# Performance work log

Hardware: AMD Instinct MI355X
Metric: run time of the kernel (lower is better)

The kernel has to match this reference:

```python
import jax, jax.numpy as jnp
import numpy as np

WEIGHT = 1e-7
SIGMA_RGB = 15.0
SIGMA_XY = 100.0
SCALE = 0.5


def _nearest_resize(x, Ho, Wo):
    # torch F.interpolate mode='nearest': src = floor(dst * in/out)
    H, W = x.shape[-2], x.shape[-1]
    iy = (jnp.arange(Ho) * (H / Ho)).astype(jnp.int32)
    ix = (jnp.arange(Wo) * (W / Wo)).astype(jnp.int32)
    return x[..., iy[:, None], ix[None, :]]


def _bilinear_resize(x, Ho, Wo):
    # torch bilinear, align_corners=False (half-pixel centers, no antialias)
    H, W = x.shape[-2], x.shape[-1]
    yc = jnp.clip((jnp.arange(Ho, dtype=jnp.float32) + 0.5) * (H / Ho) - 0.5, 0.0, H - 1.0)
    xc = jnp.clip((jnp.arange(Wo, dtype=jnp.float32) + 0.5) * (W / Wo) - 0.5, 0.0, W - 1.0)
    y0 = jnp.floor(yc).astype(jnp.int32); y1 = jnp.minimum(y0 + 1, H - 1); ty = yc - y0
    x0 = jnp.floor(xc).astype(jnp.int32); x1 = jnp.minimum(x0 + 1, W - 1); tx = xc - x0
    g = lambda yi, xi: x[..., yi[:, None], xi[None, :]]
    top = g(y0, x0) * (1.0 - tx) + g(y0, x1) * tx
    bot = g(y1, x0) * (1.0 - tx) + g(y1, x1) * tx
    return top * (1.0 - ty[:, None]) + bot * ty[:, None]


def _dense_energy(images, segmentations, ROIs, seg_label):
    N, K, H, W = segmentations.shape
    Ho, Wo = int(H * SCALE), int(W * SCALE)
    P = Ho * Wo
    img_s = _nearest_resize(images, Ho, Wo)            # [N,3,Ho,Wo]
    seg_s = _bilinear_resize(segmentations, Ho, Wo)    # [N,K,Ho,Wo]
    roi_s = _nearest_resize(ROIs, Ho, Wo)              # [N,Ho,Wo]
    lbl_s = _nearest_resize(seg_label, Ho, Wo)         # [N,1,Ho,Wo]
    unlabel = (lbl_s == 255)[:, 0]                     # [N,Ho,Wo]

    # Gate = clamp(ROI - max_k seg, min=0), with unlabeled region forced to 1
    gate = roi_s - jnp.max(seg_s, axis=1)
    gate = jnp.where(unlabel, 1.0, gate)
    gate = jnp.maximum(gate, 0.0)
    gate = jax.lax.stop_gradient(gate)                 # constant in the custom backward

    seg_roi = seg_s * roi_s[:, None]                   # [N,K,Ho,Wo]

    sxy = SIGMA_XY * SCALE
    yy, xx = jnp.meshgrid(jnp.arange(Ho, dtype=jnp.float32),
                          jnp.arange(Wo, dtype=jnp.float32), indexing='ij')
    pos = jnp.stack([xx.ravel() / sxy, yy.ravel() / sxy], axis=-1)  # [P,2]

    def per_image(img, seg):
        # img [3,Ho,Wo], seg [K,Ho,Wo] -> AS [K,P]: Gaussian bilateral filter
        col = img.reshape(img.shape[0], P).T / SIGMA_RGB            # [P,3]
        f = jnp.concatenate([pos, col], axis=-1)                    # [P,5]
        sq = jnp.sum(f * f, axis=-1)
        d2 = jnp.maximum(sq[:, None] + sq[None, :] - 2.0 * (f @ f.T), 0.0)
        Wm = jnp.exp(-0.5 * d2)                                     # [P,P] affinity
        return seg.reshape(seg.shape[0], P) @ Wm                    # symmetric Wm

    AS = jax.vmap(per_image)(img_s, seg_roi)                        # [N,K,P]
    AS = AS * gate.reshape(N, 1, P)
    loss = -jnp.sum(seg_roi.reshape(N, K, P) * AS) / N
    return (WEIGHT * loss).reshape(1)


def setup_inputs() -> dict:
    key = jax.random.key(0)
    k1, k2, k3, k4 = jax.random.split(key, 4)
    N, C, K, H, W = 4, 3, 21, 128, 128
    images = jax.random.uniform(k1, (N, C, H, W), dtype=jnp.float32) * 255.0
    segmentations = jax.nn.softmax(jax.random.normal(k2, (N, K, H, W), dtype=jnp.float32), axis=1)
    ROIs = jax.random.randint(k3, (N, H, W), 0, 2).astype(jnp.float32)
    seg_label = jax.random.randint(k4, (N, 1, H, W), 0, 256).astype(jnp.int32)
    return {"images": images, "segmentations": segmentations, "ROIs": ROIs, "seg_label": seg_label}


def reference(images, segmentations, ROIs, seg_label):
    return _dense_energy(images, segmentations, ROIs, seg_label)
```

## Files before the change

### kernel.cpp

```cpp
#include <hip/hip_runtime.h>
#include <hip/hip_bf16.h>


typedef _Float16 v8h __attribute__((ext_vector_type(8)));
typedef float v16f __attribute__((ext_vector_type(16)));

#define NIMG 4
#define KCH 21
#define HIN 128
#define WIN 128
#define PPX 4096
#define TPB 32
#define TRI 528
#define NBLK (NIMG * TRI)

#define WS_S_OFF 0x000000
#define WS_F_OFF 0x180000
#define PART_OFF 0x300000

#define LOG2E 1.44269504088896341f

__device__ __forceinline__ float fexp2(float x) {
#if __has_builtin(__builtin_amdgcn_exp2f)
    return __builtin_amdgcn_exp2f(x);
#else
    return __expf(x * 0.69314718055994531f);
#endif
}

__global__ __launch_bounds__(256) void prep_kernel(
    const float* __restrict__ img, const float* __restrict__ seg,
    const float* __restrict__ roi, const int* __restrict__ lbl,
    char* __restrict__ ws)
{
    int gid = blockIdx.x * 256 + threadIdx.x;
    int n = gid >> 12, p = gid & (PPX - 1);
    int y = p >> 6, x = p & 63, iy = 2 * y, ix = 2 * x;
    const float inv_rgb = 1.0f / 15.0f, inv_sxy = 1.0f / 50.0f;

    float rv = roi[((size_t)n * HIN + iy) * WIN + ix];
    int   lb = lbl[((size_t)n * HIN + iy) * WIN + ix];

    float sv[KCH]; float maxs = 0.0f;
    #pragma unroll
    for (int k = 0; k < KCH; k++) {
        const float* sp = seg + ((((size_t)n * KCH + k) * HIN + iy) * WIN + ix);
        float2 a = *(const float2*)sp;
        float2 c = *(const float2*)(sp + WIN);
        float s = 0.25f * (a.x + a.y + c.x + c.y);
        maxs = fmaxf(maxs, s);
        sv[k] = s * rv;
    }
    float gate = (lb == 255) ? 1.0f : fmaxf(rv - maxs, 0.0f);

    union { float4 q[6]; _Float16 e[48]; } rs;
    #pragma unroll
    for (int k = 0; k < KCH; k++) {
        _Float16 s = (_Float16)sv[k];
        rs.e[k] = (_Float16)(sv[k] * gate);
        rs.e[24 + k] = s;
    }
    #pragma unroll
    for (int k = KCH; k < 24; k++) { rs.e[k] = (_Float16)0.f; rs.e[24 + k] = (_Float16)0.f; }

    float f[5];
    f[0] = (float)x * inv_sxy;
    f[1] = (float)y * inv_sxy;
    f[2] = img[(((size_t)n * 3 + 0) * HIN + iy) * WIN + ix] * inv_rgb;
    f[3] = img[(((size_t)n * 3 + 1) * HIN + iy) * WIN + ix] * inv_rgb;
    f[4] = img[(((size_t)n * 3 + 2) * HIN + iy) * WIN + ix] * inv_rgb;

    _Float16 hi[5], lo[5];
    float sq = 0.f;
    #pragma unroll
    for (int u = 0; u < 5; u++) {
        hi[u] = (_Float16)f[u];
        lo[u] = (_Float16)(f[u] - (float)hi[u]);
        float fe = (float)hi[u] + (float)lo[u];
        sq = fmaf(fe, fe, sq);
    }
    float sqv = -0.5f * sq;
    _Float16 sqh = (_Float16)sqv;
    _Float16 sql = (_Float16)(sqv - (float)sqh);
    const _Float16 h0 = (_Float16)0.f, h1 = (_Float16)1.f;

    union { float4 q[6]; _Float16 e[48]; } rf;
    #pragma unroll
    for (int u = 0; u < 5; u++) {
        rf.e[u] = hi[u];       rf.e[8 + u] = lo[u];
        rf.e[16 + u] = hi[u];  rf.e[24 + u] = hi[u];
        rf.e[32 + u] = lo[u];  rf.e[40 + u] = lo[u];
    }
    rf.e[5] = sqh; rf.e[6] = sql; rf.e[7] = h1;
    rf.e[13] = h0; rf.e[14] = h0; rf.e[15] = h1;
    rf.e[21] = h1; rf.e[22] = h1; rf.e[23] = sqh;
    rf.e[29] = h0; rf.e[30] = h0; rf.e[31] = sql;
    rf.e[37] = h0; rf.e[38] = h0; rf.e[39] = h0;
    rf.e[45] = h0; rf.e[46] = h0; rf.e[47] = h0;

    float4* ds = (float4*)(ws + WS_S_OFF + (size_t)gid * 96);
    float4* df = (float4*)(ws + WS_F_OFF + (size_t)gid * 96);
    #pragma unroll
    for (int u = 0; u < 6; u++) { ds[u] = rs.q[u]; df[u] = rf.q[u]; }
}

#define LSTR 104
#define SREG_O 0
#define FREG_O 26624
#define RED_O  53248
#define LDS_BYTES 53280

__global__ __launch_bounds__(256)
__attribute__((amdgpu_waves_per_eu(1, 4)))
void pairs_kernel(
    const char* __restrict__ ws, float* __restrict__ part)
{
    __shared__ __align__(16) char smem[LDS_BYTES];
    int b = blockIdx.x;
    int n = b / TRI, r = b - n * TRI;
    int i = 0, rowlen = TPB;
    while (r >= rowlen) { r -= rowlen; rowlen--; i++; }
    int j = i + r;
    bool diag = (i == j);

    int t = threadIdx.x;
    int lane = t & 63, half = lane >> 5, lr = lane & 31, wv = t >> 6;
    int wq = wv & 1, wp = wv >> 1;

    {
        const float4* gsi = (const float4*)(ws + WS_S_OFF) + (size_t)(n * PPX + i * 128) * 6;
        const float4* gfi = (const float4*)(ws + WS_F_OFF) + (size_t)(n * PPX + i * 128) * 6;
        #pragma unroll
        for (int k = 0; k < 3; k++) {
            int v = t + k * 256;
            int row = v / 6, off = v - row * 6;
            float4 vs = gsi[v], vf = gfi[v];
            char* dS = smem + SREG_O + row * LSTR + off * 16;
            char* dF = smem + FREG_O + row * LSTR + off * 16;
            *(float2*)dS = make_float2(vs.x, vs.y);
            *(float2*)(dS + 8) = make_float2(vs.z, vs.w);
            *(float2*)dF = make_float2(vf.x, vf.y);
            *(float2*)(dF + 8) = make_float2(vf.z, vf.w);
        }
        if (!diag) {
            const float4* gsj = (const float4*)(ws + WS_S_OFF) + (size_t)(n * PPX + j * 128) * 6;
            const float4* gfj = (const float4*)(ws + WS_F_OFF) + (size_t)(n * PPX + j * 128) * 6;
            #pragma unroll
            for (int k = 0; k < 3; k++) {
                int v = t + k * 256;
                int row = v / 6, off = v - row * 6;
                float4 vs = gsj[v], vf = gfj[v];
                char* dS = smem + SREG_O + (128 + row) * LSTR + off * 16;
                char* dF = smem + FREG_O + (128 + row) * LSTR + off * 16;
                *(float2*)dS = make_float2(vs.x, vs.y);
                *(float2*)(dS + 8) = make_float2(vs.z, vs.w);
                *(float2*)dF = make_float2(vf.x, vf.y);
                *(float2*)(dF + 8) = make_float2(vf.z, vf.w);
            }
        }
    }
    __syncthreads();

    int jrow0 = diag ? 0 : 128;
    float acc = 0.0f;

    #pragma unroll
    for (int sp = 0; sp < 2; sp++) {
        int pr = wp * 64 + sp * 32 + lr;
        const char* sb = smem + SREG_O + pr * LSTR;
        const char* fb = smem + FREG_O + pr * LSTR;
        union { v8h h; float2 f[2]; } A0, A1, A2, Af;
        A0.f[0] = *(const float2*)(sb + half * 16);
        A0.f[1] = *(const float2*)(sb + half * 16 + 8);
        A1.f[0] = *(const float2*)(sb + 32 + half * 16);
        A1.f[1] = *(const float2*)(sb + 32 + half * 16 + 8);
        A2.f[0] = *(const float2*)(sb + 64 + half * 16);
        A2.f[1] = *(const float2*)(sb + 64 + half * 16 + 8);
        Af.f[0] = *(const float2*)(fb + half * 16);
        Af.f[1] = *(const float2*)(fb + half * 16 + 8);

        #pragma unroll
        for (int s = 0; s < 2; s++) {
            int cr = jrow0 + wq * 64 + s * 32 + lr;
            const char* cb = smem + SREG_O + cr * LSTR;
            const char* gb = smem + FREG_O + cr * LSTR;
            union { v8h h; float2 f[2]; } B0, B1, B2, Bf1, Bf2;
            B0.f[0] = *(const float2*)(cb + 48 + half * 16);
            B0.f[1] = *(const float2*)(cb + 48 + half * 16 + 8);
            int o1 = half ? 0 : 80;
            B1.f[0] = *(const float2*)(cb + o1);
            B1.f[1] = *(const float2*)(cb + o1 + 8);
            B2.f[0] = *(const float2*)(cb + 16 + half * 16);
            B2.f[1] = *(const float2*)(cb + 16 + half * 16 + 8);
            Bf1.f[0] = *(const float2*)(gb + 32 + half * 16);
            Bf1.f[1] = *(const float2*)(gb + 32 + half * 16 + 8);
            Bf2.f[0] = *(const float2*)(gb + 64 + half * 16);
            Bf2.f[1] = *(const float2*)(gb + 64 + half * 16 + 8);

            v16f z = {0.f,0.f,0.f,0.f,0.f,0.f,0.f,0.f,0.f,0.f,0.f,0.f,0.f,0.f,0.f,0.f};
            v16f c2 = __builtin_amdgcn_mfma_f32_32x32x16_f16(Af.h, Bf1.h, z, 0, 0, 0);
            c2 = __builtin_amdgcn_mfma_f32_32x32x16_f16(Af.h, Bf2.h, c2, 0, 0, 0);
            v16f c1 = __builtin_amdgcn_mfma_f32_32x32x16_f16(A0.h, B0.h, z, 0, 0, 0);
            c1 = __builtin_amdgcn_mfma_f32_32x32x16_f16(A1.h, B1.h, c1, 0, 0, 0);
            c1 = __builtin_amdgcn_mfma_f32_32x32x16_f16(A2.h, B2.h, c1, 0, 0, 0);

            #pragma unroll
            for (int rr = 0; rr < 16; rr++) {
                float arg = fminf(LOG2E * c2[rr], 0.0f);
                acc = fmaf(fexp2(arg), c1[rr], acc);
            }
        }
    }

    #pragma unroll
    for (int off = 32; off > 0; off >>= 1) acc += __shfl_down(acc, off, 64);
    float* wred = (float*)(smem + RED_O);
    if ((t & 63) == 0) wred[t >> 6] = acc;
    __syncthreads();
    if (t == 0) {
        float partial = (wred[0] + wred[1]) + (wred[2] + wred[3]);
        if (diag) partial *= 0.5f;
        part[b] = partial;
    }
}

__global__ __launch_bounds__(256) void finalize_kernel(
    const float* __restrict__ part, float* __restrict__ out)
{
    __shared__ float s[256];
    int t = threadIdx.x;
    float v = 0.f;
    #pragma unroll
    for (int k = 0; k < 9; k++) {
        int idx = t + k * 256;
        if (idx < NBLK) v += part[idx];
    }
    s[t] = v;
    __syncthreads();
    #pragma unroll
    for (int off = 128; off > 0; off >>= 1) {
        if (t < off) s[t] += s[t + off];
        __syncthreads();
    }
    if (t == 0) out[0] = s[0] * (-1e-7f / (float)NIMG);
}

extern "C" void kernel_launch(void* const* d_in, const int* in_sizes, int n_in,
                              void* d_out, int out_size, void* d_ws, size_t ws_size,
                              hipStream_t stream) {
    const float* images = (const float*)d_in[0];
    const float* seg    = (const float*)d_in[1];
    const float* rois   = (const float*)d_in[2];
    const int*   lbl    = (const int*)d_in[3];
    float* out = (float*)d_out;
    char*  ws  = (char*)d_ws;
    float* part = (float*)(ws + PART_OFF);

    hipLaunchKernelGGL(prep_kernel, dim3((NIMG * PPX) / 256), dim3(256), 0, stream,
                       images, seg, rois, lbl, ws);
    hipLaunchKernelGGL(pairs_kernel, dim3(NBLK), dim3(256), 0, stream,
                       (const char*)ws, part);
    hipLaunchKernelGGL(finalize_kernel, dim3(1), dim3(256), 0, stream,
                       (const float*)part, out);
}
```

Measured before the change: 85.18 us.

## Compact feature workspace, rebuild B operands in-register, fuse finalize via last-block atomic

Shrinks the per-pixel feature record from 96 to 32 bytes, and reconstructs the two B-side feature MFMA operands in registers from the compact hi/lo rows using lane-dependent selects. This cuts global and LDS traffic and lowers the LDS footprint, which may allow more blocks per CU. The separate finalize kernel is removed: each pairs block atomically increments a counter and the last block performs the final reduction, saving one launch. The exp-accumulate chain is also split into four independent accumulators to shorten the dependency chain.

```diff
diff --git a/kernel.cpp b/kernel.cpp
--- a/kernel.cpp
+++ b/kernel.cpp
@@ -16,7 +16,8 @@
 
 #define WS_S_OFF 0x000000
 #define WS_F_OFF 0x180000
-#define PART_OFF 0x300000
+#define PART_OFF 0x200000
+#define CNT_OFF  0x202200
 
 #define LOG2E 1.44269504088896341f
 
@@ -34,6 +35,7 @@
     char* __restrict__ ws)
 {
     int gid = blockIdx.x * 256 + threadIdx.x;
+    if (gid == 0) *(unsigned*)(ws + CNT_OFF) = 0u;
     int n = gid >> 12, p = gid & (PPX - 1);
     int y = p >> 6, x = p & 63, iy = 2 * y, ix = 2 * x;
     const float inv_rgb = 1.0f / 15.0f, inv_sxy = 1.0f / 50.0f;
@@ -56,9 +58,8 @@
     union { float4 q[6]; _Float16 e[48]; } rs;
     #pragma unroll
     for (int k = 0; k < KCH; k++) {
-        _Float16 s = (_Float16)sv[k];
         rs.e[k] = (_Float16)(sv[k] * gate);
-        rs.e[24 + k] = s;
+        rs.e[24 + k] = (_Float16)sv[k];
     }
     #pragma unroll
     for (int k = KCH; k < 24; k++) { rs.e[k] = (_Float16)0.f; rs.e[24 + k] = (_Float16)0.f; }
@@ -84,36 +85,32 @@
     _Float16 sql = (_Float16)(sqv - (float)sqh);
     const _Float16 h0 = (_Float16)0.f, h1 = (_Float16)1.f;
 
-    union { float4 q[6]; _Float16 e[48]; } rf;
-    #pragma unroll
-    for (int u = 0; u < 5; u++) {
-        rf.e[u] = hi[u];       rf.e[8 + u] = lo[u];
-        rf.e[16 + u] = hi[u];  rf.e[24 + u] = hi[u];
-        rf.e[32 + u] = lo[u];  rf.e[40 + u] = lo[u];
-    }
+    union { float4 q[2]; _Float16 e[16]; } rf;
+    #pragma unroll
+    for (int u = 0; u < 5; u++) { rf.e[u] = hi[u]; rf.e[8 + u] = lo[u]; }
     rf.e[5] = sqh; rf.e[6] = sql; rf.e[7] = h1;
     rf.e[13] = h0; rf.e[14] = h0; rf.e[15] = h1;
-    rf.e[21] = h1; rf.e[22] = h1; rf.e[23] = sqh;
-    rf.e[29] = h0; rf.e[30] = h0; rf.e[31] = sql;
-    rf.e[37] = h0; rf.e[38] = h0; rf.e[39] = h0;
-    rf.e[45] = h0; rf.e[46] = h0; rf.e[47] = h0;
 
     float4* ds = (float4*)(ws + WS_S_OFF + (size_t)gid * 96);
-    float4* df = (float4*)(ws + WS_F_OFF + (size_t)gid * 96);
-    #pragma unroll
-    for (int u = 0; u < 6; u++) { ds[u] = rs.q[u]; df[u] = rf.q[u]; }
+    #pragma unroll
+    for (int u = 0; u < 6; u++) ds[u] = rs.q[u];
+    float4* df = (float4*)(ws + WS_F_OFF + (size_t)gid * 32);
+    df[0] = rf.q[0]; df[1] = rf.q[1];
 }
 
 #define LSTR 104
+#define FSTR 40
 #define SREG_O 0
 #define FREG_O 26624
-#define RED_O  53248
-#define LDS_BYTES 53280
+#define RED_O  36864
+#define FLAG_O 36880
+#define LDS_BYTES 36896
 
 __global__ __launch_bounds__(256)
 __attribute__((amdgpu_waves_per_eu(1, 4)))
 void pairs_kernel(
-    const char* __restrict__ ws, float* __restrict__ part)
+    const char* __restrict__ ws, float* __restrict__ part,
+    unsigned* __restrict__ cnt, float* __restrict__ out)
 {
     __shared__ __align__(16) char smem[LDS_BYTES];
     int b = blockIdx.x;
@@ -129,46 +126,53 @@
 
     {
         const float4* gsi = (const float4*)(ws + WS_S_OFF) + (size_t)(n * PPX + i * 128) * 6;
-        const float4* gfi = (const float4*)(ws + WS_F_OFF) + (size_t)(n * PPX + i * 128) * 6;
         #pragma unroll
         for (int k = 0; k < 3; k++) {
             int v = t + k * 256;
             int row = v / 6, off = v - row * 6;
-            float4 vs = gsi[v], vf = gfi[v];
+            float4 vs = gsi[v];
             char* dS = smem + SREG_O + row * LSTR + off * 16;
-            char* dF = smem + FREG_O + row * LSTR + off * 16;
             *(float2*)dS = make_float2(vs.x, vs.y);
             *(float2*)(dS + 8) = make_float2(vs.z, vs.w);
+        }
+        const float4* gfi = (const float4*)(ws + WS_F_OFF) + (size_t)(n * PPX + i * 128) * 2;
+        {
+            int row = t >> 1, off = t & 1;
+            float4 vf = gfi[t];
+            char* dF = smem + FREG_O + row * FSTR + off * 16;
             *(float2*)dF = make_float2(vf.x, vf.y);
             *(float2*)(dF + 8) = make_float2(vf.z, vf.w);
         }
         if (!diag) {
             const float4* gsj = (const float4*)(ws + WS_S_OFF) + (size_t)(n * PPX + j * 128) * 6;
-            const float4* gfj = (const float4*)(ws + WS_F_OFF) + (size_t)(n * PPX + j * 128) * 6;
             #pragma unroll
             for (int k = 0; k < 3; k++) {
                 int v = t + k * 256;
                 int row = v / 6, off = v - row * 6;
-                float4 vs = gsj[v], vf = gfj[v];
+                float4 vs = gsj[v];
                 char* dS = smem + SREG_O + (128 + row) * LSTR + off * 16;
-                char* dF = smem + FREG_O + (128 + row) * LSTR + off * 16;
                 *(float2*)dS = make_float2(vs.x, vs.y);
                 *(float2*)(dS + 8) = make_float2(vs.z, vs.w);
-                *(float2*)dF = make_float2(vf.x, vf.y);
-                *(float2*)(dF + 8) = make_float2(vf.z, vf.w);
             }
+            const float4* gfj = (const float4*)(ws + WS_F_OFF) + (size_t)(n * PPX + j * 128) * 2;
+            int row = t >> 1, off = t & 1;
+            float4 vf = gfj[t];
+            char* dF = smem + FREG_O + (128 + row) * FSTR + off * 16;
+            *(float2*)dF = make_float2(vf.x, vf.y);
+            *(float2*)(dF + 8) = make_float2(vf.z, vf.w);
         }
     }
     __syncthreads();
 
     int jrow0 = diag ? 0 : 128;
-    float acc = 0.0f;
+    const _Float16 selA = half ? (_Float16)0.f : (_Float16)1.f;
+    float ac0 = 0.f, ac1 = 0.f, ac2 = 0.f, ac3 = 0.f;
 
     #pragma unroll
     for (int sp = 0; sp < 2; sp++) {
         int pr = wp * 64 + sp * 32 + lr;
         const char* sb = smem + SREG_O + pr * LSTR;
-        const char* fb = smem + FREG_O + pr * LSTR;
+        const char* fb = smem + FREG_O + pr * FSTR;
         union { v8h h; float2 f[2]; } A0, A1, A2, Af;
         A0.f[0] = *(const float2*)(sb + half * 16);
         A0.f[1] = *(const float2*)(sb + half * 16 + 8);
@@ -183,8 +187,9 @@
         for (int s = 0; s < 2; s++) {
             int cr = jrow0 + wq * 64 + s * 32 + lr;
             const char* cb = smem + SREG_O + cr * LSTR;
-            const char* gb = smem + FREG_O + cr * LSTR;
-            union { v8h h; float2 f[2]; } B0, B1, B2, Bf1, Bf2;
+            const char* gb = smem + FREG_O + cr * FSTR;
+            union { v8h h; float2 f[2]; } B0, B1, B2;
+            union { v8h h; float2 f[2]; _Float16 e[8]; } U, L;
             B0.f[0] = *(const float2*)(cb + 48 + half * 16);
             B0.f[1] = *(const float2*)(cb + 48 + half * 16 + 8);
             int o1 = half ? 0 : 80;
@@ -192,10 +197,15 @@
             B1.f[1] = *(const float2*)(cb + o1 + 8);
             B2.f[0] = *(const float2*)(cb + 16 + half * 16);
             B2.f[1] = *(const float2*)(cb + 16 + half * 16 + 8);
-            Bf1.f[0] = *(const float2*)(gb + 32 + half * 16);
-            Bf1.f[1] = *(const float2*)(gb + 32 + half * 16 + 8);
-            Bf2.f[0] = *(const float2*)(gb + 64 + half * 16);
-            Bf2.f[1] = *(const float2*)(gb + 64 + half * 16 + 8);
+            U.f[0] = *(const float2*)(gb);      U.f[1] = *(const float2*)(gb + 8);
+            L.f[0] = *(const float2*)(gb + 16); L.f[1] = *(const float2*)(gb + 24);
+
+            union { v8h h; _Float16 e[8]; } Bf1, Bf2;
+            Bf1.h = U.h;
+            Bf1.e[5] = selA; Bf1.e[6] = selA;
+            Bf1.e[7] = half ? U.e[6] : U.e[5];
+            Bf2.h = L.h;
+            Bf2.e[7] = (_Float16)0.f;
 
             v16f z = {0.f,0.f,0.f,0.f,0.f,0.f,0.f,0.f,0.f,0.f,0.f,0.f,0.f,0.f,0.f,0.f};
             v16f c2 = __builtin_amdgcn_mfma_f32_32x32x16_f16(Af.h, Bf1.h, z, 0, 0, 0);
@@ -207,42 +217,52 @@
             #pragma unroll
             for (int rr = 0; rr < 16; rr++) {
                 float arg = fminf(LOG2E * c2[rr], 0.0f);
-                acc = fmaf(fexp2(arg), c1[rr], acc);
+                float w = fexp2(arg);
+                if ((rr & 3) == 0)      ac0 = fmaf(w, c1[rr], ac0);
+                else if ((rr & 3) == 1) ac1 = fmaf(w, c1[rr], ac1);
+                else if ((rr & 3) == 2) ac2 = fmaf(w, c1[rr], ac2);
+                else                    ac3 = fmaf(w, c1[rr], ac3);
             }
         }
     }
 
+    float acc = (ac0 + ac1) + (ac2 + ac3);
     #pragma unroll
     for (int off = 32; off > 0; off >>= 1) acc += __shfl_down(acc, off, 64);
     float* wred = (float*)(smem + RED_O);
+    int* flag = (int*)(smem + FLAG_O);
     if ((t & 63) == 0) wred[t >> 6] = acc;
     __syncthreads();
     if (t == 0) {
         float partial = (wred[0] + wred[1]) + (wred[2] + wred[3]);
         if (diag) partial *= 0.5f;
         part[b] = partial;
-    }
-}
-
-__global__ __launch_bounds__(256) void finalize_kernel(
-    const float* __restrict__ part, float* __restrict__ out)
-{
-    __shared__ float s[256];
-    int t = threadIdx.x;
-    float v = 0.f;
-    #pragma unroll
-    for (int k = 0; k < 9; k++) {
-        int idx = t + k * 256;
-        if (idx < NBLK) v += part[idx];
-    }
-    s[t] = v;
+        __threadfence();
+        unsigned old = atomicAdd(cnt, 1u);
+        *flag = (old == NBLK - 1) ? 1 : 0;
+    }
     __syncthreads();
-    #pragma unroll
-    for (int off = 128; off > 0; off >>= 1) {
-        if (t < off) s[t] += s[t + off];
+
+    if (*flag) {
+        __threadfence();
+        float v = 0.f;
+        #pragma unroll
+        for (int k = 0; k < 9; k++) {
+            int idx = t + k * 256;
+            if (idx < NBLK)
+                v += __hip_atomic_load(&part[idx], __ATOMIC_RELAXED,
+                                       __HIP_MEMORY_SCOPE_AGENT);
+        }
+        float* red = (float*)smem;
+        red[t] = v;
         __syncthreads();
-    }
-    if (t == 0) out[0] = s[0] * (-1e-7f / (float)NIMG);
+        #pragma unroll
+        for (int off = 128; off > 0; off >>= 1) {
+            if (t < off) red[t] += red[t + off];
+            __syncthreads();
+        }
+        if (t == 0) out[0] = red[0] * (-1e-7f / (float)NIMG);
+    }
 }
 
 extern "C" void kernel_launch(void* const* d_in, const int* in_sizes, int n_in,
@@ -255,11 +275,10 @@
     float* out = (float*)d_out;
     char*  ws  = (char*)d_ws;
     float* part = (float*)(ws + PART_OFF);
+    unsigned* cnt = (unsigned*)(ws + CNT_OFF);
 
     hipLaunchKernelGGL(prep_kernel, dim3((NIMG * PPX) / 256), dim3(256), 0, stream,
                        images, seg, rois, lbl, ws);
     hipLaunchKernelGGL(pairs_kernel, dim3(NBLK), dim3(256), 0, stream,
-                       (const char*)ws, part);
-    hipLaunchKernelGGL(finalize_kernel, dim3(1), dim3(256), 0, stream,
-                       (const float*)part, out);
-}
+                       (const char*)ws, part, cnt, out);
+}
```

Measured after the change: 115.0 us. 1.35x slower.
